# Kernel optimization log

Hardware: AMD Instinct MI355X
Metric: run time of the kernel (lower is better)

## Reference

```python
import jax, jax.numpy as jnp
import numpy as np

H = 512

def setup_inputs() -> dict:
    key = jax.random.key(0)
    ks = jax.random.split(key, 10)
    T, B, S = 64, 8, 512
    scale = 1.0 / np.sqrt(H)
    return {
        "attn_dec_state": jax.random.normal(ks[0], (T, B, H), jnp.float32),
        "attn_enc_state": jax.random.normal(ks[1], (S, B, H), jnp.float32),
        "attn_coverage": jax.random.uniform(ks[2], (B, S), jnp.float32),
        "Wq": jax.random.normal(ks[3], (H, H), jnp.float32) * scale,   # linear_query weight (in,out)
        "bq": jnp.zeros((H,), jnp.float32),
        "Wc": jax.random.normal(ks[4], (H, H), jnp.float32) * scale,   # linear_context weight
        "v": jax.random.normal(ks[5], (H,), jnp.float32) * scale,       # v projection H->1
        "Wo": jax.random.normal(ks[6], (2 * H, H), jnp.float32) * scale,  # linear_out weight
        "bo": jnp.zeros((H,), jnp.float32),
        "wcov": jax.random.normal(ks[7], (H,), jnp.float32) * scale,    # linear_cover weight 1->H
    }

def reference(attn_dec_state, attn_enc_state, attn_coverage, Wq, bq, Wc, v, Wo, bo, wcov):
    dec = jnp.transpose(attn_dec_state, (1, 0, 2))   # [B,T,H]
    enc = jnp.transpose(attn_enc_state, (1, 0, 2))   # [B,S,H]
    # coverage: linear_cover(1->H) applied to each scalar, added to enc, then tanh
    enc = jnp.tanh(enc + attn_coverage[:, :, None] * wcov)  # [B,S,H]
    # additive (Bahdanau) score with broadcast-tanh
    a1 = jnp.einsum('bth,hk->btk', dec, Wq) + bq             # [B,T,H]
    a2 = jnp.einsum('bsh,hk->bsk', enc, Wc)                  # [B,S,H]
    scores = jnp.einsum('btsh,h->bts', jnp.tanh(a1[:, :, None, :] + a2[:, None, :, :]), v)  # [B,T,S]
    align = jax.nn.softmax(scores, axis=-1)                  # [B,T,S]
    c = jnp.einsum('bts,bsh->bth', align, enc)               # [B,T,H]
    concat = jnp.concatenate([c, dec], axis=-1)              # [B,T,2H]
    attn_h = jnp.einsum('btd,dk->btk', concat, Wo) + bo      # [B,T,H]
    attn_h = jnp.transpose(attn_h, (1, 0, 2))                # [T,B,H]
    align_out = jnp.transpose(align, (1, 0, 2))              # [T,B,S]
    return attn_h, align_out
```

## Files before the change

### kernel.cpp

```cpp
#include <hip/hip_runtime.h>
#include <cstddef>

static constexpr int TT = 64;
static constexpr int BB = 8;
static constexpr int SS = 512;
static constexpr int HH = 512;

typedef __attribute__((ext_vector_type(8))) short bf16x8;
typedef __attribute__((ext_vector_type(4))) float f32x4;

__device__ __forceinline__ float fast_tanh(float x) {
  float e = __expf(2.0f * x);
  return 1.0f - 2.0f * __builtin_amdgcn_rcpf(e + 1.0f);
}
__device__ __forceinline__ unsigned short f2bf(float f) {
  unsigned u = __float_as_uint(f);
  return (unsigned short)((u + 0x7FFFu + ((u >> 16) & 1u)) >> 16);
}

__global__ __launch_bounds__(256)
void k_prep(const float* __restrict__ enc, const float* __restrict__ cov,
            const float* __restrict__ wcov, const float* __restrict__ dec,
            const float* __restrict__ Wq, const float* __restrict__ Wc,
            const float* __restrict__ Wo,
            unsigned short* __restrict__ encpb, unsigned short* __restrict__ concatb,
            unsigned short* __restrict__ WqT, unsigned short* __restrict__ WcT,
            unsigned short* __restrict__ WoT) {
  __shared__ float tile[32][33];
  const int blk = blockIdx.x, tid = threadIdx.x;

  if (blk < 2048) {
    const int r = tid >> 7, c = (tid & 127) * 4;
    const int bs = blk * 2 + r;
    const int s = bs & 511, b = bs >> 9;
    const float4 ev = *(const float4*)(enc + (size_t)(s * BB + b) * HH + c);
    const float cv = cov[bs];
    const float4 wv = *(const float4*)(wcov + c);
    ushort4 o;
    o.x = f2bf(fast_tanh(ev.x + cv * wv.x));
    o.y = f2bf(fast_tanh(ev.y + cv * wv.y));
    o.z = f2bf(fast_tanh(ev.z + cv * wv.z));
    o.w = f2bf(fast_tanh(ev.w + cv * wv.w));
    *(ushort4*)(encpb + (size_t)bs * HH + c) = o;
  } else if (blk < 2304) {
    const int r = tid >> 7, c = (tid & 127) * 4;
    const int m = (blk - 2048) * 2 + r, t = m & 63, b = m >> 6;
    const float4 dv = *(const float4*)(dec + (size_t)(t * BB + b) * HH + c);
    ushort4 o;
    o.x = f2bf(dv.x); o.y = f2bf(dv.y); o.z = f2bf(dv.z); o.w = f2bf(dv.w);
    *(ushort4*)(concatb + (size_t)m * 1024 + 512 + c) = o;
  } else {
    int l = blk - 2304;
    const float* W; unsigned short* WT; int KT;
    if (l < 256)      { W = Wq; WT = WqT; KT = 512; }
    else if (l < 512) { W = Wc; WT = WcT; KT = 512; l -= 256; }
    else              { W = Wo; WT = WoT; KT = 1024; l -= 512; }
    const int n0 = (l & 15) * 32, k0 = (l >> 4) * 32;
    const int r = tid >> 3, c4 = (tid & 7) * 4;
    const float4 w = *(const float4*)(W + (size_t)(k0 + r) * 512 + n0 + c4);
    tile[r][c4 + 0] = w.x; tile[r][c4 + 1] = w.y;
    tile[r][c4 + 2] = w.z; tile[r][c4 + 3] = w.w;
    __syncthreads();
    unsigned short* o = WT + (size_t)(n0 + r) * KT + k0 + c4;
#pragma unroll
    for (int i = 0; i < 4; ++i) o[i] = f2bf(tile[c4 + i][r]);
  }
}

template<int LDA, int LDB>
__device__ __forceinline__ void gemm_tile(const unsigned short* __restrict__ A,
                                          const unsigned short* __restrict__ BT,
                                          int m0, int n0, int kbeg, int kend,
                                          unsigned short (*As)[72],
                                          unsigned short (*Bs)[72],
                                          f32x4 acc[4]) {
  const int tid = threadIdx.x, w = tid >> 6, lane = tid & 63;
  const int lr = tid >> 2, lk = (tid & 3) * 16;
  const int fm = w * 16 + (lane & 15), fk = (lane >> 4) * 8;
  for (int k0 = kbeg; k0 < kend; k0 += 64) {
    const uint4* ga = (const uint4*)(A + (size_t)(m0 + lr) * LDA + k0 + lk);
    const uint4* gb = (const uint4*)(BT + (size_t)(n0 + lr) * LDB + k0 + lk);
    uint4 a0 = ga[0], a1 = ga[1], b0 = gb[0], b1 = gb[1];
    *(uint4*)&As[lr][lk] = a0;  *(uint4*)&As[lr][lk + 8] = a1;
    *(uint4*)&Bs[lr][lk] = b0;  *(uint4*)&Bs[lr][lk + 8] = b1;
    __syncthreads();
#pragma unroll
    for (int ks = 0; ks < 2; ++ks) {
      bf16x8 af = *(const bf16x8*)&As[fm][ks * 32 + fk];
#pragma unroll
      for (int j = 0; j < 4; ++j) {
        bf16x8 bf = *(const bf16x8*)&Bs[j * 16 + (lane & 15)][ks * 32 + fk];
        acc[j] = __builtin_amdgcn_mfma_f32_16x16x32_bf16(af, bf, acc[j], 0, 0, 0);
      }
    }
    __syncthreads();
  }
}

__global__ __launch_bounds__(256)
void k_gemm12(const unsigned short* __restrict__ concatb,
              const unsigned short* __restrict__ encpb,
              const unsigned short* __restrict__ WqT,
              const unsigned short* __restrict__ WcT,
              const unsigned short* __restrict__ WoT,
              const float* __restrict__ bq, const float* __restrict__ bo,
              float* __restrict__ Ea1, unsigned short* __restrict__ Ea2b,
              float* __restrict__ attn_h) {
  __shared__ unsigned short As[64][72];
  __shared__ unsigned short Bs[64][72];
  const int g = blockIdx.x, tid = threadIdx.x;
  const int w = tid >> 6, lane = tid & 63;
  const int col = lane & 15, rq = lane >> 4;

  if (g < 64) {
    const int m0 = (g >> 3) * 64, n0 = (g & 7) * 64;
    f32x4 acc[4] = {};
    gemm_tile<1024, 512>(concatb + 512, WqT, m0, n0, 0, 512, As, Bs, acc);
#pragma unroll
    for (int j = 0; j < 4; ++j) {
      const int n = n0 + j * 16 + col;
      const float bv = bq[n];
#pragma unroll
      for (int r = 0; r < 4; ++r) {
        const int m = m0 + w * 16 + rq * 4 + r;
        float val = fminf(fmaxf(acc[j][r] + bv, -10.5f), 10.5f);
        Ea1[(size_t)m * 512 + n] = __expf(2.0f * val);
      }
    }
  } else if (g < 576) {
    const int u = g - 64;
    const int m0 = (u >> 3) * 64, n0 = (u & 7) * 64;
    f32x4 acc[4] = {};
    gemm_tile<512, 512>(encpb, WcT, m0, n0, 0, 512, As, Bs, acc);
#pragma unroll
    for (int j = 0; j < 4; ++j) {
      const int n = n0 + j * 16 + col;
#pragma unroll
      for (int r = 0; r < 4; ++r) {
        const int m = m0 + w * 16 + rq * 4 + r;
        float val = fminf(fmaxf(acc[j][r], -10.5f), 10.5f);
        Ea2b[(size_t)m * 512 + n] = f2bf(__expf(2.0f * val));
      }
    }
  } else {
    const int u = g - 576;
    const int m0 = (u >> 3) * 64, n0 = (u & 7) * 64;
    f32x4 acc[4] = {};
    gemm_tile<1024, 1024>(concatb, WoT, m0, n0, 512, 1024, As, Bs, acc);
#pragma unroll
    for (int j = 0; j < 4; ++j) {
      const int n = n0 + j * 16 + col;
      const float bv = bo[n];
#pragma unroll
      for (int r = 0; r < 4; ++r) {
        const int m = m0 + w * 16 + rq * 4 + r;
        const int bi = m >> 6, t = m & 63;
        attn_h[(size_t)(t * BB + bi) * 512 + n] = acc[j][r] + bv;
      }
    }
  }
}

__global__ __launch_bounds__(1024)
void k_attn(const float* __restrict__ Ea1, const unsigned short* __restrict__ Ea2b,
            const float* __restrict__ v, const unsigned short* __restrict__ encpb,
            float* __restrict__ align_out, unsigned short* __restrict__ concatb) {
  __shared__ __align__(16) char smem[20544];
  float (*sc)[512]   = (float(*)[512])smem;
  float (*ea1s)[512] = (float(*)[512])(smem + 4096);
  float* v2s         = (float*)(smem + 12288);
  float2* part       = (float2*)(smem + 4096);
  float (*red)[8]    = (float(*)[8])(smem + 20480);

  const int g = blockIdx.x, tid = threadIdx.x;
  const int b = g & 7, t0 = (g >> 3) * 2;
  const int wv = tid >> 6, lane = tid & 63;
  const int hq = lane & 3, sl = lane >> 2;

  if (tid < 512) {
    ea1s[0][tid] = Ea1[(size_t)(b * TT + t0) * HH + tid];
    ea1s[1][tid] = Ea1[(size_t)(b * TT + t0 + 1) * HH + tid];
  } else {
    v2s[tid - 512] = 2.0f * v[tid - 512];
  }
  __syncthreads();

  const int s0 = wv * 32 + sl;
  {
    const unsigned short* e2r0 = Ea2b + (size_t)(b * SS + s0) * HH;
    const unsigned short* e2r1 = e2r0 + (size_t)16 * HH;
    float acc[2][2] = {};
#define BFLO(u) __uint_as_float((u) << 16)
#define BFHI(u) __uint_as_float((u) & 0xffff0000u)
#define PAIR(E1a, E2a, Va, E1b, E2b, Vb, A)                                  \
    {                                                                        \
      const float x1 = fmaf(E1a, E2a, 1.0f), x2 = fmaf(E1b, E2b, 1.0f);      \
      const float rr = __builtin_amdgcn_rcpf(x1 * x2);                       \
      const float nn = fmaf(Va, x2, Vb * x1);                                \
      A = fmaf(nn, rr, A);                                                   \
    }
#pragma unroll 4
    for (int it = 0; it < 16; ++it) {
      const int h = it * 32 + hq * 8;
      const uint4 u0 = *(const uint4*)(e2r0 + h);
      const uint4 u1 = *(const uint4*)(e2r1 + h);
      const float4 va = *(const float4*)&v2s[h];
      const float4 vb = *(const float4*)&v2s[h + 4];
      float4 e1a[2], e1b[2];
      e1a[0] = *(const float4*)&ea1s[0][h]; e1b[0] = *(const float4*)&ea1s[0][h + 4];
      e1a[1] = *(const float4*)&ea1s[1][h]; e1b[1] = *(const float4*)&ea1s[1][h + 4];
#pragma unroll
      for (int i = 0; i < 2; ++i) {
        PAIR(e1a[i].x, BFLO(u0.x), va.x, e1a[i].y, BFHI(u0.x), va.y, acc[i][0]);
        PAIR(e1a[i].z, BFLO(u0.y), va.z, e1a[i].w, BFHI(u0.y), va.w, acc[i][0]);
        PAIR(e1b[i].x, BFLO(u0.z), vb.x, e1b[i].y, BFHI(u0.z), vb.y, acc[i][0]);
        PAIR(e1b[i].z, BFLO(u0.w), vb.z, e1b[i].w, BFHI(u0.w), vb.w, acc[i][0]);
        PAIR(e1a[i].x, BFLO(u1.x), va.x, e1a[i].y, BFHI(u1.x), va.y, acc[i][1]);
        PAIR(e1a[i].z, BFLO(u1.y), va.z, e1a[i].w, BFHI(u1.y), va.w, acc[i][1]);
        PAIR(e1b[i].x, BFLO(u1.z), vb.x, e1b[i].y, BFHI(u1.z), vb.y, acc[i][1]);
        PAIR(e1b[i].z, BFLO(u1.w), vb.z, e1b[i].w, BFHI(u1.w), vb.w, acc[i][1]);
      }
    }
#undef PAIR
#undef BFLO
#undef BFHI
#pragma unroll
    for (int i = 0; i < 2; ++i)
#pragma unroll
      for (int j = 0; j < 2; ++j) {
        acc[i][j] += __shfl_xor(acc[i][j], 1);
        acc[i][j] += __shfl_xor(acc[i][j], 2);
      }
    if (hq == 0) {
      sc[0][s0] = -acc[0][0]; sc[0][s0 + 16] = -acc[0][1];
      sc[1][s0] = -acc[1][0]; sc[1][s0 + 16] = -acc[1][1];
    }
  }
  __syncthreads();

  float x0 = 0.f, x1 = 0.f, e0 = 0.f, e1 = 0.f;
  if (tid < 512) {
    x0 = sc[0][tid]; x1 = sc[1][tid];
    float m0 = x0, m1 = x1;
#pragma unroll
    for (int off = 32; off; off >>= 1) {
      m0 = fmaxf(m0, __shfl_xor(m0, off));
      m1 = fmaxf(m1, __shfl_xor(m1, off));
    }
    if (lane == 0) { red[0][wv] = m0; red[1][wv] = m1; }
  }
  __syncthreads();
  {
    float m0 = red[0][0], m1 = red[1][0];
#pragma unroll
    for (int w2 = 1; w2 < 8; ++w2) { m0 = fmaxf(m0, red[0][w2]); m1 = fmaxf(m1, red[1][w2]); }
    __syncthreads();
    if (tid < 512) {
      e0 = __expf(x0 - m0); e1 = __expf(x1 - m1);
      float s0v = e0, s1v = e1;
#pragma unroll
      for (int off = 32; off; off >>= 1) {
        s0v += __shfl_xor(s0v, off);
        s1v += __shfl_xor(s1v, off);
      }
      if (lane == 0) { red[0][wv] = s0v; red[1][wv] = s1v; }
    }
  }
  __syncthreads();
  {
    float sum0 = 0.f, sum1 = 0.f;
#pragma unroll
    for (int w2 = 0; w2 < 8; ++w2) { sum0 += red[0][w2]; sum1 += red[1][w2]; }
    if (tid < 512) {
      const float a0 = e0 * __builtin_amdgcn_rcpf(sum0);
      const float a1 = e1 * __builtin_amdgcn_rcpf(sum1);
      align_out[(size_t)(t0 + 0) * BB * SS + b * SS + tid] = a0;
      align_out[(size_t)(t0 + 1) * BB * SS + b * SS + tid] = a1;
      sc[0][tid] = a0;
      sc[1][tid] = a1;
    }
  }
  __syncthreads();

  {
    const int q = tid >> 8, hp = tid & 255;
    const unsigned* ep = (const unsigned*)encpb + (size_t)b * SS * 256;
    float c00 = 0.f, c01 = 0.f, c10 = 0.f, c11 = 0.f;
#pragma unroll 8
    for (int s2 = q * 128; s2 < q * 128 + 128; ++s2) {
      const unsigned u = ep[s2 * 256 + hp];
      const float elo = __uint_as_float(u << 16);
      const float ehi = __uint_as_float(u & 0xffff0000u);
      const float av0 = sc[0][s2], av1 = sc[1][s2];
      c00 = fmaf(av0, elo, c00); c01 = fmaf(av0, ehi, c01);
      c10 = fmaf(av1, elo, c10); c11 = fmaf(av1, ehi, c11);
    }
    part[(0 * 4 + q) * 256 + hp] = make_float2(c00, c01);
    part[(1 * 4 + q) * 256 + hp] = make_float2(c10, c11);
  }
  __syncthreads();
  if (tid < 512) {
    const int t = tid >> 8, hp = tid & 255;
    float clo = 0.f, chi = 0.f;
#pragma unroll
    for (int q = 0; q < 4; ++q) {
      const float2 p = part[(t * 4 + q) * 256 + hp];
      clo += p.x; chi += p.y;
    }
    ((unsigned*)concatb)[(size_t)(b * TT + t0 + t) * 512 + hp] =
        (unsigned)f2bf(clo) | ((unsigned)f2bf(chi) << 16);
  }
}

__global__ __launch_bounds__(256)
void k_out(const unsigned short* __restrict__ A,
           const unsigned short* __restrict__ BT,
           float* __restrict__ C) {
  __shared__ unsigned short As[64][72];
  __shared__ unsigned short Bs[64][72];
  const int tid = threadIdx.x;
  const int w = tid >> 6, lane = tid & 63;
  const int tau = blockIdx.x >> 2, kc = blockIdx.x & 3;
  const int n0 = (tau & 7) * 64, m0 = (tau >> 3) * 64;

  f32x4 acc[4] = {};
  gemm_tile<1024, 1024>(A, BT, m0, n0, kc * 128, kc * 128 + 128, As, Bs, acc);

  const int col = lane & 15, rq = lane >> 4;
#pragma unroll
  for (int j = 0; j < 4; ++j) {
    const int n = n0 + j * 16 + col;
#pragma unroll
    for (int r = 0; r < 4; ++r) {
      const int m = m0 + w * 16 + rq * 4 + r;
      const int bi = m >> 6, t = m & 63;
      unsafeAtomicAdd(&C[(size_t)(t * BB + bi) * 512 + n], acc[j][r]);
    }
  }
}

extern "C" void kernel_launch(void* const* d_in, const int* in_sizes, int n_in,
                              void* d_out, int out_size, void* d_ws, size_t ws_size,
                              hipStream_t stream) {
  const float* dec  = (const float*)d_in[0];
  const float* enc  = (const float*)d_in[1];
  const float* cov  = (const float*)d_in[2];
  const float* Wq   = (const float*)d_in[3];
  const float* bq   = (const float*)d_in[4];
  const float* Wc   = (const float*)d_in[5];
  const float* v    = (const float*)d_in[6];
  const float* Wo   = (const float*)d_in[7];
  const float* bo   = (const float*)d_in[8];
  const float* wcov = (const float*)d_in[9];

  float* out = (float*)d_out;
  float* attn_h    = out;
  float* align_out = out + (size_t)TT * BB * HH;

  char* w = (char*)d_ws;
  const size_t MB = 1024 * 1024;
  unsigned short* encpb   = (unsigned short*)(w);
  unsigned short* WqT     = (unsigned short*)(w + 4 * MB);
  unsigned short* WcT     = (unsigned short*)(w + 4 * MB + 512 * 1024);
  unsigned short* WoT     = (unsigned short*)(w + 5 * MB);
  unsigned short* concatb = (unsigned short*)(w + 6 * MB);
  float*          Ea1     = (float*)(w + 7 * MB);
  unsigned short* Ea2b    = (unsigned short*)(w + 8 * MB);

  k_prep<<<3328, 256, 0, stream>>>(enc, cov, wcov, dec, Wq, Wc, Wo,
                                   encpb, concatb, WqT, WcT, WoT);
  k_gemm12<<<640, 256, 0, stream>>>(concatb, encpb, WqT, WcT, WoT, bq, bo,
                                    Ea1, Ea2b, attn_h);
  k_attn<<<256, 1024, 0, stream>>>(Ea1, Ea2b, v, encpb, align_out, concatb);
  k_out<<<256, 256, 0, stream>>>(concatb, WoT, attn_h);
}
```

Before: 124.6 us.

## Fuse four kernels into one cooperative persistent kernel with grid syncs

Replaces the four-launch pipeline (prep, projection GEMMs, attention, output GEMM) with a single cooperative kernel of 256 blocks of 1024 threads, separated by grid.sync barriers. Each batch index gets its own replicated copy of the transposed bf16 weights, so the later GEMMs read a per-batch copy. The aim is to remove launch gaps and inter-kernel tails. In exchange it adds grid-wide barriers, extra weight-transpose writes for the replicas, and idle sub-blocks during the GEMM phases. If the cooperative launch fails, the code falls back to the original four-kernel path.

Result: slower. 243.0 us (+95.1%).

```diff
diff --git a/kernel.cpp b/kernel.cpp
--- a/kernel.cpp
+++ b/kernel.cpp
@@ -1,5 +1,8 @@
 #include <hip/hip_runtime.h>
+#include <hip/hip_cooperative_groups.h>
 #include <cstddef>
+
+namespace cg = cooperative_groups;
 
 static constexpr int TT = 64;
 static constexpr int BB = 8;
@@ -16,6 +19,332 @@
 __device__ __forceinline__ unsigned short f2bf(float f) {
   unsigned u = __float_as_uint(f);
   return (unsigned short)((u + 0x7FFFu + ((u >> 16) & 1u)) >> 16);
+}
+
+template<int LDA, int LDB>
+__device__ __forceinline__ void gemm_tile(const unsigned short* __restrict__ A,
+                                          const unsigned short* __restrict__ BT,
+                                          int m0, int n0, int kbeg, int kend,
+                                          unsigned short (*As)[72],
+                                          unsigned short (*Bs)[72],
+                                          f32x4 acc[4], int tid) {
+  const int w = tid >> 6, lane = tid & 63;
+  const int lr = tid >> 2, lk = (tid & 3) * 16;
+  const int fm = w * 16 + (lane & 15), fk = (lane >> 4) * 8;
+  for (int k0 = kbeg; k0 < kend; k0 += 64) {
+    const uint4* ga = (const uint4*)(A + (size_t)(m0 + lr) * LDA + k0 + lk);
+    const uint4* gb = (const uint4*)(BT + (size_t)(n0 + lr) * LDB + k0 + lk);
+    uint4 a0 = ga[0], a1 = ga[1], b0 = gb[0], b1 = gb[1];
+    *(uint4*)&As[lr][lk] = a0;  *(uint4*)&As[lr][lk + 8] = a1;
+    *(uint4*)&Bs[lr][lk] = b0;  *(uint4*)&Bs[lr][lk + 8] = b1;
+    __syncthreads();
+#pragma unroll
+    for (int ks = 0; ks < 2; ++ks) {
+      bf16x8 af = *(const bf16x8*)&As[fm][ks * 32 + fk];
+#pragma unroll
+      for (int j = 0; j < 4; ++j) {
+        bf16x8 bf = *(const bf16x8*)&Bs[j * 16 + (lane & 15)][ks * 32 + fk];
+        acc[j] = __builtin_amdgcn_mfma_f32_16x16x32_bf16(af, bf, acc[j], 0, 0, 0);
+      }
+    }
+    __syncthreads();
+  }
+}
+
+__global__ __launch_bounds__(1024)
+void k_fused(const float* __restrict__ dec, const float* __restrict__ enc,
+             const float* __restrict__ cov, const float* __restrict__ Wq,
+             const float* __restrict__ bq, const float* __restrict__ Wc,
+             const float* __restrict__ v, const float* __restrict__ Wo,
+             const float* __restrict__ bo, const float* __restrict__ wcov,
+             unsigned short* __restrict__ encpb, unsigned short* __restrict__ concatb,
+             float* __restrict__ Ea1, unsigned short* __restrict__ Ea2b,
+             unsigned short* __restrict__ wrepl,
+             float* __restrict__ attn_h, float* __restrict__ align_out) {
+  __shared__ __align__(16) char smem[82944];
+  cg::grid_group grid = cg::this_grid();
+
+  const int blk = blockIdx.x, tid = threadIdx.x;
+  const int b = blk & 7, i = blk >> 3;
+  unsigned short* WR = wrepl + (size_t)b * (1024u * 1024u);
+  const unsigned short* WqT = WR;
+  const unsigned short* WcT = WR + 256 * 1024;
+  const unsigned short* WoT = WR + 512 * 1024;
+
+  {
+    const int c = (tid & 127) * 4;
+#pragma unroll
+    for (int rep = 0; rep < 2; ++rep) {
+      const int s = i * 16 + (tid >> 7) + rep * 8;
+      const float4 ev = *(const float4*)(enc + (size_t)(s * BB + b) * HH + c);
+      const float cv = cov[b * SS + s];
+      const float4 wvv = *(const float4*)(wcov + c);
+      ushort4 o;
+      o.x = f2bf(fast_tanh(ev.x + cv * wvv.x));
+      o.y = f2bf(fast_tanh(ev.y + cv * wvv.y));
+      o.z = f2bf(fast_tanh(ev.z + cv * wvv.z));
+      o.w = f2bf(fast_tanh(ev.w + cv * wvv.w));
+      *(ushort4*)(encpb + (size_t)(b * SS + s) * HH + c) = o;
+    }
+    if (tid < 256) {
+      const int t = i * 2 + (tid >> 7);
+      const int c2 = (tid & 127) * 4;
+      const float4 dv = *(const float4*)(dec + (size_t)(t * BB + b) * HH + c2);
+      ushort4 o;
+      o.x = f2bf(dv.x); o.y = f2bf(dv.y); o.z = f2bf(dv.z); o.w = f2bf(dv.w);
+      *(ushort4*)(concatb + (size_t)(b * 64 + t) * 1024 + 512 + c2) = o;
+    }
+    const int sub = tid >> 8, st = tid & 255;
+    float (*tile)[33] = (float(*)[33])(smem + sub * 4224);
+    const int r = st >> 3, c4 = (st & 7) * 4;
+    for (int it = 0; it < 8; ++it) {
+      int l = it * 128 + i * 4 + sub;
+      const float* W; unsigned short* WT; int KT;
+      if (l < 256)      { W = Wq; WT = WR;              KT = 512; }
+      else if (l < 512) { W = Wc; WT = WR + 256 * 1024; KT = 512;  l -= 256; }
+      else              { W = Wo; WT = WR + 512 * 1024; KT = 1024; l -= 512; }
+      const int n0 = (l & 15) * 32, k0 = (l >> 4) * 32;
+      const float4 w4 = *(const float4*)(W + (size_t)(k0 + r) * 512 + n0 + c4);
+      tile[r][c4 + 0] = w4.x; tile[r][c4 + 1] = w4.y;
+      tile[r][c4 + 2] = w4.z; tile[r][c4 + 3] = w4.w;
+      __syncthreads();
+      unsigned short* o = WT + (size_t)(n0 + r) * KT + k0 + c4;
+#pragma unroll
+      for (int ii = 0; ii < 4; ++ii) o[ii] = f2bf(tile[c4 + ii][r]);
+      __syncthreads();
+    }
+  }
+  grid.sync();
+
+  {
+    const int sub = tid >> 8, st = tid & 255;
+    unsigned short (*As)[72] = (unsigned short(*)[72])(smem + sub * 18432);
+    unsigned short (*Bs)[72] = (unsigned short(*)[72])(smem + sub * 18432 + 9216);
+    const int w4 = st >> 6, lane = st & 63;
+    const int col = lane & 15, rq = lane >> 4;
+    if (sub < 2) {
+      const int rem = i * 2 + sub;
+      const int m0 = b * 512 + (rem & 7) * 64, n0 = (rem >> 3) * 64;
+      f32x4 acc[4] = {};
+      gemm_tile<512, 512>(encpb, WcT, m0, n0, 0, 512, As, Bs, acc, st);
+#pragma unroll
+      for (int j = 0; j < 4; ++j) {
+        const int n = n0 + j * 16 + col;
+#pragma unroll
+        for (int r = 0; r < 4; ++r) {
+          const int m = m0 + w4 * 16 + rq * 4 + r;
+          float val = fminf(fmaxf(acc[j][r], -10.5f), 10.5f);
+          Ea2b[(size_t)m * 512 + n] = f2bf(__expf(2.0f * val));
+        }
+      }
+    } else if (sub == 2 && i < 8) {
+      const int m0 = b * 64, n0 = i * 64;
+      f32x4 acc[4] = {};
+      gemm_tile<1024, 512>(concatb + 512, WqT, m0, n0, 0, 512, As, Bs, acc, st);
+#pragma unroll
+      for (int j = 0; j < 4; ++j) {
+        const int n = n0 + j * 16 + col;
+        const float bv = bq[n];
+#pragma unroll
+        for (int r = 0; r < 4; ++r) {
+          const int m = m0 + w4 * 16 + rq * 4 + r;
+          float val = fminf(fmaxf(acc[j][r] + bv, -10.5f), 10.5f);
+          Ea1[(size_t)m * 512 + n] = __expf(2.0f * val);
+        }
+      }
+    } else if (sub == 2 && i < 16) {
+      const int m0 = b * 64, n0 = (i - 8) * 64;
+      f32x4 acc[4] = {};
+      gemm_tile<1024, 1024>(concatb, WoT, m0, n0, 512, 1024, As, Bs, acc, st);
+#pragma unroll
+      for (int j = 0; j < 4; ++j) {
+        const int n = n0 + j * 16 + col;
+        const float bv = bo[n];
+#pragma unroll
+        for (int r = 0; r < 4; ++r) {
+          const int m = m0 + w4 * 16 + rq * 4 + r;
+          const int t = m & 63;
+          attn_h[(size_t)(t * BB + b) * 512 + n] = acc[j][r] + bv;
+        }
+      }
+    } else {
+      for (int q = 0; q < 16; ++q) __syncthreads();
+    }
+  }
+  grid.sync();
+
+  {
+    float (*sc)[512]   = (float(*)[512])smem;
+    float (*ea1s)[512] = (float(*)[512])(smem + 4096);
+    float* v2s         = (float*)(smem + 12288);
+    float2* part       = (float2*)(smem + 4096);
+    float (*red)[8]    = (float(*)[8])(smem + 20480);
+
+    const int t0 = i * 2;
+    const int wvA = tid >> 6, lane = tid & 63;
+    const int hq = lane & 3, sl = lane >> 2;
+
+    if (tid < 512) {
+      ea1s[0][tid] = Ea1[(size_t)(b * TT + t0) * HH + tid];
+      ea1s[1][tid] = Ea1[(size_t)(b * TT + t0 + 1) * HH + tid];
+    } else {
+      v2s[tid - 512] = 2.0f * v[tid - 512];
+    }
+    __syncthreads();
+
+    const int s0 = wvA * 32 + sl;
+    {
+      const unsigned short* e2r0 = Ea2b + (size_t)(b * SS + s0) * HH;
+      const unsigned short* e2r1 = e2r0 + (size_t)16 * HH;
+      float acc[2][2] = {};
+#define BFLO(u) __uint_as_float((u) << 16)
+#define BFHI(u) __uint_as_float((u) & 0xffff0000u)
+#define PAIR(E1a, E2a, Va, E1b, E2b, Vb, A)                                  \
+      {                                                                      \
+        const float x1 = fmaf(E1a, E2a, 1.0f), x2 = fmaf(E1b, E2b, 1.0f);    \
+        const float rr = __builtin_amdgcn_rcpf(x1 * x2);                     \
+        const float nn = fmaf(Va, x2, Vb * x1);                              \
+        A = fmaf(nn, rr, A);                                                 \
+      }
+#pragma unroll 4
+      for (int it = 0; it < 16; ++it) {
+        const int h = it * 32 + hq * 8;
+        const uint4 u0 = *(const uint4*)(e2r0 + h);
+        const uint4 u1 = *(const uint4*)(e2r1 + h);
+        const float4 va = *(const float4*)&v2s[h];
+        const float4 vb = *(const float4*)&v2s[h + 4];
+        float4 e1a[2], e1b[2];
+        e1a[0] = *(const float4*)&ea1s[0][h]; e1b[0] = *(const float4*)&ea1s[0][h + 4];
+        e1a[1] = *(const float4*)&ea1s[1][h]; e1b[1] = *(const float4*)&ea1s[1][h + 4];
+#pragma unroll
+        for (int ii = 0; ii < 2; ++ii) {
+          PAIR(e1a[ii].x, BFLO(u0.x), va.x, e1a[ii].y, BFHI(u0.x), va.y, acc[ii][0]);
+          PAIR(e1a[ii].z, BFLO(u0.y), va.z, e1a[ii].w, BFHI(u0.y), va.w, acc[ii][0]);
+          PAIR(e1b[ii].x, BFLO(u0.z), vb.x, e1b[ii].y, BFHI(u0.z), vb.y, acc[ii][0]);
+          PAIR(e1b[ii].z, BFLO(u0.w), vb.z, e1b[ii].w, BFHI(u0.w), vb.w, acc[ii][0]);
+          PAIR(e1a[ii].x, BFLO(u1.x), va.x, e1a[ii].y, BFHI(u1.x), va.y, acc[ii][1]);
+          PAIR(e1a[ii].z, BFLO(u1.y), va.z, e1a[ii].w, BFHI(u1.y), va.w, acc[ii][1]);
+          PAIR(e1b[ii].x, BFLO(u1.z), vb.x, e1b[ii].y, BFHI(u1.z), vb.y, acc[ii][1]);
+          PAIR(e1b[ii].z, BFLO(u1.w), vb.z, e1b[ii].w, BFHI(u1.w), vb.w, acc[ii][1]);
+        }
+      }
+#undef PAIR
+#undef BFLO
+#undef BFHI
+#pragma unroll
+      for (int ii = 0; ii < 2; ++ii)
+#pragma unroll
+        for (int j = 0; j < 2; ++j) {
+          acc[ii][j] += __shfl_xor(acc[ii][j], 1);
+          acc[ii][j] += __shfl_xor(acc[ii][j], 2);
+        }
+      if (hq == 0) {
+        sc[0][s0] = -acc[0][0]; sc[0][s0 + 16] = -acc[0][1];
+        sc[1][s0] = -acc[1][0]; sc[1][s0 + 16] = -acc[1][1];
+      }
+    }
+    __syncthreads();
+
+    float x0 = 0.f, x1 = 0.f, e0 = 0.f, e1 = 0.f;
+    if (tid < 512) {
+      x0 = sc[0][tid]; x1 = sc[1][tid];
+      float m0 = x0, m1 = x1;
+#pragma unroll
+      for (int off = 32; off; off >>= 1) {
+        m0 = fmaxf(m0, __shfl_xor(m0, off));
+        m1 = fmaxf(m1, __shfl_xor(m1, off));
+      }
+      if (lane == 0) { red[0][wvA] = m0; red[1][wvA] = m1; }
+    }
+    __syncthreads();
+    {
+      float m0 = red[0][0], m1 = red[1][0];
+#pragma unroll
+      for (int w2 = 1; w2 < 8; ++w2) { m0 = fmaxf(m0, red[0][w2]); m1 = fmaxf(m1, red[1][w2]); }
+      __syncthreads();
+      if (tid < 512) {
+        e0 = __expf(x0 - m0); e1 = __expf(x1 - m1);
+        float s0v = e0, s1v = e1;
+#pragma unroll
+        for (int off = 32; off; off >>= 1) {
+          s0v += __shfl_xor(s0v, off);
+          s1v += __shfl_xor(s1v, off);
+        }
+        if (lane == 0) { red[0][wvA] = s0v; red[1][wvA] = s1v; }
+      }
+    }
+    __syncthreads();
+    {
+      float sum0 = 0.f, sum1 = 0.f;
+#pragma unroll
+      for (int w2 = 0; w2 < 8; ++w2) { sum0 += red[0][w2]; sum1 += red[1][w2]; }
+      if (tid < 512) {
+        const float a0 = e0 * __builtin_amdgcn_rcpf(sum0);
+        const float a1 = e1 * __builtin_amdgcn_rcpf(sum1);
+        align_out[(size_t)(t0 + 0) * BB * SS + b * SS + tid] = a0;
+        align_out[(size_t)(t0 + 1) * BB * SS + b * SS + tid] = a1;
+        sc[0][tid] = a0;
+        sc[1][tid] = a1;
+      }
+    }
+    __syncthreads();
+
+    {
+      const int q = tid >> 8, hp = tid & 255;
+      const unsigned* ep = (const unsigned*)encpb + (size_t)b * SS * 256;
+      float c00 = 0.f, c01 = 0.f, c10 = 0.f, c11 = 0.f;
+#pragma unroll 8
+      for (int s2 = q * 128; s2 < q * 128 + 128; ++s2) {
+        const unsigned u = ep[s2 * 256 + hp];
+        const float elo = __uint_as_float(u << 16);
+        const float ehi = __uint_as_float(u & 0xffff0000u);
+        const float av0 = sc[0][s2], av1 = sc[1][s2];
+        c00 = fmaf(av0, elo, c00); c01 = fmaf(av0, ehi, c01);
+        c10 = fmaf(av1, elo, c10); c11 = fmaf(av1, ehi, c11);
+      }
+      part[(0 * 4 + q) * 256 + hp] = make_float2(c00, c01);
+      part[(1 * 4 + q) * 256 + hp] = make_float2(c10, c11);
+    }
+    __syncthreads();
+    if (tid < 512) {
+      const int t = tid >> 8, hp = tid & 255;
+      float clo = 0.f, chi = 0.f;
+#pragma unroll
+      for (int q = 0; q < 4; ++q) {
+        const float2 p = part[(t * 4 + q) * 256 + hp];
+        clo += p.x; chi += p.y;
+      }
+      ((unsigned*)concatb)[(size_t)(b * TT + t0 + t) * 512 + hp] =
+          (unsigned)f2bf(clo) | ((unsigned)f2bf(chi) << 16);
+    }
+  }
+  grid.sync();
+
+  {
+    const int sub = tid >> 8, st = tid & 255;
+    if (sub < 2) {
+      unsigned short (*As)[72] = (unsigned short(*)[72])(smem + sub * 18432);
+      unsigned short (*Bs)[72] = (unsigned short(*)[72])(smem + sub * 18432 + 9216);
+      const int ntile = (blk >> 3) & 7, kc = (blk >> 6) * 2 + sub;
+      const int m0 = b * 64, n0 = ntile * 64;
+      f32x4 acc[4] = {};
+      gemm_tile<1024, 1024>(concatb, WoT, m0, n0, kc * 64, kc * 64 + 64, As, Bs, acc, st);
+      const int w4 = st >> 6, lane = st & 63;
+      const int col = lane & 15, rq = lane >> 4;
+#pragma unroll
+      for (int j = 0; j < 4; ++j) {
+        const int n = n0 + j * 16 + col;
+#pragma unroll
+        for (int r = 0; r < 4; ++r) {
+          const int m = m0 + w4 * 16 + rq * 4 + r;
+          const int t = m & 63;
+          unsafeAtomicAdd(&attn_h[(size_t)(t * BB + b) * 512 + n], acc[j][r]);
+        }
+      }
+    } else {
+      __syncthreads(); __syncthreads();
+    }
+  }
 }
 
 __global__ __launch_bounds__(256)
@@ -67,36 +396,6 @@
   }
 }
 
-template<int LDA, int LDB>
-__device__ __forceinline__ void gemm_tile(const unsigned short* __restrict__ A,
-                                          const unsigned short* __restrict__ BT,
-                                          int m0, int n0, int kbeg, int kend,
-                                          unsigned short (*As)[72],
-                                          unsigned short (*Bs)[72],
-                                          f32x4 acc[4]) {
-  const int tid = threadIdx.x, w = tid >> 6, lane = tid & 63;
-  const int lr = tid >> 2, lk = (tid & 3) * 16;
-  const int fm = w * 16 + (lane & 15), fk = (lane >> 4) * 8;
-  for (int k0 = kbeg; k0 < kend; k0 += 64) {
-    const uint4* ga = (const uint4*)(A + (size_t)(m0 + lr) * LDA + k0 + lk);
-    const uint4* gb = (const uint4*)(BT + (size_t)(n0 + lr) * LDB + k0 + lk);
-    uint4 a0 = ga[0], a1 = ga[1], b0 = gb[0], b1 = gb[1];
-    *(uint4*)&As[lr][lk] = a0;  *(uint4*)&As[lr][lk + 8] = a1;
-    *(uint4*)&Bs[lr][lk] = b0;  *(uint4*)&Bs[lr][lk + 8] = b1;
-    __syncthreads();
-#pragma unroll
-    for (int ks = 0; ks < 2; ++ks) {
-      bf16x8 af = *(const bf16x8*)&As[fm][ks * 32 + fk];
-#pragma unroll
-      for (int j = 0; j < 4; ++j) {
-        bf16x8 bf = *(const bf16x8*)&Bs[j * 16 + (lane & 15)][ks * 32 + fk];
-        acc[j] = __builtin_amdgcn_mfma_f32_16x16x32_bf16(af, bf, acc[j], 0, 0, 0);
-      }
-    }
-    __syncthreads();
-  }
-}
-
 __global__ __launch_bounds__(256)
 void k_gemm12(const unsigned short* __restrict__ concatb,
               const unsigned short* __restrict__ encpb,
@@ -115,7 +414,7 @@
   if (g < 64) {
     const int m0 = (g >> 3) * 64, n0 = (g & 7) * 64;
     f32x4 acc[4] = {};
-    gemm_tile<1024, 512>(concatb + 512, WqT, m0, n0, 0, 512, As, Bs, acc);
+    gemm_tile<1024, 512>(concatb + 512, WqT, m0, n0, 0, 512, As, Bs, acc, tid);
 #pragma unroll
     for (int j = 0; j < 4; ++j) {
       const int n = n0 + j * 16 + col;
@@ -131,7 +430,7 @@
     const int u = g - 64;
     const int m0 = (u >> 3) * 64, n0 = (u & 7) * 64;
     f32x4 acc[4] = {};
-    gemm_tile<512, 512>(encpb, WcT, m0, n0, 0, 512, As, Bs, acc);
+    gemm_tile<512, 512>(encpb, WcT, m0, n0, 0, 512, As, Bs, acc, tid);
 #pragma unroll
     for (int j = 0; j < 4; ++j) {
       const int n = n0 + j * 16 + col;
@@ -146,7 +445,7 @@
     const int u = g - 576;
     const int m0 = (u >> 3) * 64, n0 = (u & 7) * 64;
     f32x4 acc[4] = {};
-    gemm_tile<1024, 1024>(concatb, WoT, m0, n0, 512, 1024, As, Bs, acc);
+    gemm_tile<1024, 1024>(concatb, WoT, m0, n0, 512, 1024, As, Bs, acc, tid);
 #pragma unroll
     for (int j = 0; j < 4; ++j) {
       const int n = n0 + j * 16 + col;
@@ -324,7 +623,7 @@
   const int n0 = (tau & 7) * 64, m0 = (tau >> 3) * 64;
 
   f32x4 acc[4] = {};
-  gemm_tile<1024, 1024>(A, BT, m0, n0, kc * 128, kc * 128 + 128, As, Bs, acc);
+  gemm_tile<1024, 1024>(A, BT, m0, n0, kc * 128, kc * 128 + 128, As, Bs, acc, tid);
 
   const int col = lane & 15, rq = lane >> 4;
 #pragma unroll
@@ -359,18 +658,33 @@
 
   char* w = (char*)d_ws;
   const size_t MB = 1024 * 1024;
+
   unsigned short* encpb   = (unsigned short*)(w);
-  unsigned short* WqT     = (unsigned short*)(w + 4 * MB);
-  unsigned short* WcT     = (unsigned short*)(w + 4 * MB + 512 * 1024);
-  unsigned short* WoT     = (unsigned short*)(w + 5 * MB);
-  unsigned short* concatb = (unsigned short*)(w + 6 * MB);
-  float*          Ea1     = (float*)(w + 7 * MB);
-  unsigned short* Ea2b    = (unsigned short*)(w + 8 * MB);
+  unsigned short* concatb = (unsigned short*)(w + 4 * MB);
+  float*          Ea1     = (float*)(w + 5 * MB);
+  unsigned short* Ea2b    = (unsigned short*)(w + 6 * MB);
+  unsigned short* wrepl   = (unsigned short*)(w + 16 * MB);
+
+  void* args[] = {(void*)&dec, (void*)&enc, (void*)&cov, (void*)&Wq, (void*)&bq,
+                  (void*)&Wc, (void*)&v, (void*)&Wo, (void*)&bo, (void*)&wcov,
+                  (void*)&encpb, (void*)&concatb, (void*)&Ea1, (void*)&Ea2b,
+                  (void*)&wrepl, (void*)&attn_h, (void*)&align_out};
+  hipError_t e = hipLaunchCooperativeKernel((const void*)k_fused, dim3(256),
+                                            dim3(1024), args, 0, stream);
+  if (e == hipSuccess) return;
+
+  unsigned short* encpbL   = (unsigned short*)(w);
+  unsigned short* WqT      = (unsigned short*)(w + 4 * MB);
+  unsigned short* WcT      = (unsigned short*)(w + 4 * MB + 512 * 1024);
+  unsigned short* WoT      = (unsigned short*)(w + 5 * MB);
+  unsigned short* concatbL = (unsigned short*)(w + 6 * MB);
+  float*          Ea1L     = (float*)(w + 7 * MB);
+  unsigned short* Ea2bL    = (unsigned short*)(w + 8 * MB);
 
   k_prep<<<3328, 256, 0, stream>>>(enc, cov, wcov, dec, Wq, Wc, Wo,
-                                   encpb, concatb, WqT, WcT, WoT);
-  k_gemm12<<<640, 256, 0, stream>>>(concatb, encpb, WqT, WcT, WoT, bq, bo,
-                                    Ea1, Ea2b, attn_h);
-  k_attn<<<256, 1024, 0, stream>>>(Ea1, Ea2b, v, encpb, align_out, concatb);
-  k_out<<<256, 256, 0, stream>>>(concatb, WoT, attn_h);
-}
+                                   encpbL, concatbL, WqT, WcT, WoT);
+  k_gemm12<<<640, 256, 0, stream>>>(concatbL, encpbL, WqT, WcT, WoT, bq, bo,
+                                    Ea1L, Ea2bL, attn_h);
+  k_attn<<<256, 1024, 0, stream>>>(Ea1L, Ea2bL, v, encpbL, align_out, concatbL);
+  k_out<<<256, 256, 0, stream>>>(concatbL, WoT, attn_h);
+}
```

## Fuse context-to-output projection into attention kernel, drop separate output GEMM

Applied to the files above, without the earlier changes.

The separate k_out GEMM, which multiplied the bf16 context by the first half of WoT using MFMA and atomic adds, is removed. k_attn now keeps the fp32 context in shared memory and each thread computes one output column as a scalar dot product against a WoT row, adding it into attn_h directly. This saves a kernel launch, the bf16 round trip of the context through global memory, and the atomics. In exchange each block rereads 512 WoT rows (512 KB of bf16) per pair of timesteps, using scalar FMAs instead of matrix cores, which puts more load on L2 and ALUs.

Result: slower. 145.5 us (+16.8%).

```diff
diff --git a/kernel.cpp b/kernel.cpp
--- a/kernel.cpp
+++ b/kernel.cpp
@@ -17,6 +17,8 @@
   unsigned u = __float_as_uint(f);
   return (unsigned short)((u + 0x7FFFu + ((u >> 16) & 1u)) >> 16);
 }
+__device__ __forceinline__ float bflo(unsigned u) { return __uint_as_float(u << 16); }
+__device__ __forceinline__ float bfhi(unsigned u) { return __uint_as_float(u & 0xffff0000u); }
 
 __global__ __launch_bounds__(256)
 void k_prep(const float* __restrict__ enc, const float* __restrict__ cov,
@@ -164,13 +166,15 @@
 __global__ __launch_bounds__(1024)
 void k_attn(const float* __restrict__ Ea1, const unsigned short* __restrict__ Ea2b,
             const float* __restrict__ v, const unsigned short* __restrict__ encpb,
-            float* __restrict__ align_out, unsigned short* __restrict__ concatb) {
-  __shared__ __align__(16) char smem[20544];
+            const unsigned short* __restrict__ WoT,
+            float* __restrict__ align_out, float* __restrict__ attn_h) {
+  __shared__ __align__(16) char smem[24640];
   float (*sc)[512]   = (float(*)[512])smem;
   float (*ea1s)[512] = (float(*)[512])(smem + 4096);
   float* v2s         = (float*)(smem + 12288);
   float2* part       = (float2*)(smem + 4096);
   float (*red)[8]    = (float(*)[8])(smem + 20480);
+  float* cs          = (float*)(smem + 20544);
 
   const int g = blockIdx.x, tid = threadIdx.x;
   const int b = g & 7, t0 = (g >> 3) * 2;
@@ -190,8 +194,6 @@
     const unsigned short* e2r0 = Ea2b + (size_t)(b * SS + s0) * HH;
     const unsigned short* e2r1 = e2r0 + (size_t)16 * HH;
     float acc[2][2] = {};
-#define BFLO(u) __uint_as_float((u) << 16)
-#define BFHI(u) __uint_as_float((u) & 0xffff0000u)
 #define PAIR(E1a, E2a, Va, E1b, E2b, Vb, A)                                  \
     {                                                                        \
       const float x1 = fmaf(E1a, E2a, 1.0f), x2 = fmaf(E1b, E2b, 1.0f);      \
@@ -211,19 +213,17 @@
       e1a[1] = *(const float4*)&ea1s[1][h]; e1b[1] = *(const float4*)&ea1s[1][h + 4];
 #pragma unroll
       for (int i = 0; i < 2; ++i) {
-        PAIR(e1a[i].x, BFLO(u0.x), va.x, e1a[i].y, BFHI(u0.x), va.y, acc[i][0]);
-        PAIR(e1a[i].z, BFLO(u0.y), va.z, e1a[i].w, BFHI(u0.y), va.w, acc[i][0]);
-        PAIR(e1b[i].x, BFLO(u0.z), vb.x, e1b[i].y, BFHI(u0.z), vb.y, acc[i][0]);
-        PAIR(e1b[i].z, BFLO(u0.w), vb.z, e1b[i].w, BFHI(u0.w), vb.w, acc[i][0]);
-        PAIR(e1a[i].x, BFLO(u1.x), va.x, e1a[i].y, BFHI(u1.x), va.y, acc[i][1]);
-        PAIR(e1a[i].z, BFLO(u1.y), va.z, e1a[i].w, BFHI(u1.y), va.w, acc[i][1]);
-        PAIR(e1b[i].x, BFLO(u1.z), vb.x, e1b[i].y, BFHI(u1.z), vb.y, acc[i][1]);
-        PAIR(e1b[i].z, BFLO(u1.w), vb.z, e1b[i].w, BFHI(u1.w), vb.w, acc[i][1]);
+        PAIR(e1a[i].x, bflo(u0.x), va.x, e1a[i].y, bfhi(u0.x), va.y, acc[i][0]);
+        PAIR(e1a[i].z, bflo(u0.y), va.z, e1a[i].w, bfhi(u0.y), va.w, acc[i][0]);
+        PAIR(e1b[i].x, bflo(u0.z), vb.x, e1b[i].y, bfhi(u0.z), vb.y, acc[i][0]);
+        PAIR(e1b[i].z, bflo(u0.w), vb.z, e1b[i].w, bfhi(u0.w), vb.w, acc[i][0]);
+        PAIR(e1a[i].x, bflo(u1.x), va.x, e1a[i].y, bfhi(u1.x), va.y, acc[i][1]);
+        PAIR(e1a[i].z, bflo(u1.y), va.z, e1a[i].w, bfhi(u1.y), va.w, acc[i][1]);
+        PAIR(e1b[i].x, bflo(u1.z), vb.x, e1b[i].y, bfhi(u1.z), vb.y, acc[i][1]);
+        PAIR(e1b[i].z, bflo(u1.w), vb.z, e1b[i].w, bfhi(u1.w), vb.w, acc[i][1]);
       }
     }
 #undef PAIR
-#undef BFLO
-#undef BFHI
 #pragma unroll
     for (int i = 0; i < 2; ++i)
 #pragma unroll
@@ -289,8 +289,8 @@
 #pragma unroll 8
     for (int s2 = q * 128; s2 < q * 128 + 128; ++s2) {
       const unsigned u = ep[s2 * 256 + hp];
-      const float elo = __uint_as_float(u << 16);
-      const float ehi = __uint_as_float(u & 0xffff0000u);
+      const float elo = bflo(u);
+      const float ehi = bfhi(u);
       const float av0 = sc[0][s2], av1 = sc[1][s2];
       c00 = fmaf(av0, elo, c00); c01 = fmaf(av0, ehi, c01);
       c10 = fmaf(av1, elo, c10); c11 = fmaf(av1, ehi, c11);
@@ -307,35 +307,28 @@
       const float2 p = part[(t * 4 + q) * 256 + hp];
       clo += p.x; chi += p.y;
     }
-    ((unsigned*)concatb)[(size_t)(b * TT + t0 + t) * 512 + hp] =
-        (unsigned)f2bf(clo) | ((unsigned)f2bf(chi) << 16);
-  }
-}
-
-__global__ __launch_bounds__(256)
-void k_out(const unsigned short* __restrict__ A,
-           const unsigned short* __restrict__ BT,
-           float* __restrict__ C) {
-  __shared__ unsigned short As[64][72];
-  __shared__ unsigned short Bs[64][72];
-  const int tid = threadIdx.x;
-  const int w = tid >> 6, lane = tid & 63;
-  const int tau = blockIdx.x >> 2, kc = blockIdx.x & 3;
-  const int n0 = (tau & 7) * 64, m0 = (tau >> 3) * 64;
-
-  f32x4 acc[4] = {};
-  gemm_tile<1024, 1024>(A, BT, m0, n0, kc * 128, kc * 128 + 128, As, Bs, acc);
-
-  const int col = lane & 15, rq = lane >> 4;
-#pragma unroll
-  for (int j = 0; j < 4; ++j) {
-    const int n = n0 + j * 16 + col;
-#pragma unroll
-    for (int r = 0; r < 4; ++r) {
-      const int m = m0 + w * 16 + rq * 4 + r;
-      const int bi = m >> 6, t = m & 63;
-      unsafeAtomicAdd(&C[(size_t)(t * BB + bi) * 512 + n], acc[j][r]);
-    }
+    cs[t * 512 + hp * 2]     = clo;
+    cs[t * 512 + hp * 2 + 1] = chi;
+  }
+  __syncthreads();
+
+  {
+    const int t = tid >> 9, n = tid & 511;
+    const unsigned short* wr = WoT + (size_t)n * 1024;
+    const float* ct = cs + t * 512;
+    float acc = 0.f;
+#pragma unroll 8
+    for (int h = 0; h < 512; h += 8) {
+      const uint4 u = *(const uint4*)(wr + h);
+      const float4 c0 = *(const float4*)(ct + h);
+      const float4 c1 = *(const float4*)(ct + h + 4);
+      acc = fmaf(c0.x, bflo(u.x), acc); acc = fmaf(c0.y, bfhi(u.x), acc);
+      acc = fmaf(c0.z, bflo(u.y), acc); acc = fmaf(c0.w, bfhi(u.y), acc);
+      acc = fmaf(c1.x, bflo(u.z), acc); acc = fmaf(c1.y, bfhi(u.z), acc);
+      acc = fmaf(c1.z, bflo(u.w), acc); acc = fmaf(c1.w, bfhi(u.w), acc);
+    }
+    const size_t oi = (size_t)((t0 + t) * BB + b) * 512 + n;
+    attn_h[oi] += acc;
   }
 }
 
@@ -371,6 +364,5 @@
                                    encpb, concatb, WqT, WcT, WoT);
   k_gemm12<<<640, 256, 0, stream>>>(concatb, encpb, WqT, WcT, WoT, bq, bo,
                                     Ea1, Ea2b, attn_h);
-  k_attn<<<256, 1024, 0, stream>>>(Ea1, Ea2b, v, encpb, align_out, concatb);
-  k_out<<<256, 256, 0, stream>>>(concatb, WoT, attn_h);
-}
+  k_attn<<<256, 1024, 0, stream>>>(Ea1, Ea2b, v, encpb, WoT, align_out, attn_h);
+}
```
